# Kernel tuning notes

Hardware: AMD Instinct MI355X
Metric: run time of the kernel (lower is better)

Reference implementation:

```python
import jax, jax.numpy as jnp
import numpy as np

EPS = 1e-6
H = 8  # number of heads


def _ln(x, a, b):
    # Custom LayerNorm from the source: uses unbiased std and divides by (std + eps)
    m = x.mean(-1, keepdims=True)
    s = x.std(-1, keepdims=True, ddof=1)
    return a * (x - m) / (s + EPS) + b


def setup_inputs() -> dict:
    key = jax.random.key(0)
    L, B, S, D, F = 6, 8, 1024, 512, 2048
    ks = jax.random.split(key, 8)
    sc = 0.02  # param init scale
    return {
        "x": jax.random.normal(ks[0], (B, S, D), jnp.float32),
        "mask": jnp.ones((B, 1, S), jnp.int32),
        "Wqkv": (jax.random.normal(ks[1], (L, 4, D, D), jnp.float32) * sc),
        "bqkv": jnp.zeros((L, 4, D), jnp.float32),
        "W1": (jax.random.normal(ks[2], (L, D, F), jnp.float32) * sc),
        "b1": jnp.zeros((L, F), jnp.float32),
        "W2": (jax.random.normal(ks[3], (L, F, D), jnp.float32) * sc),
        "b2": jnp.zeros((L, D), jnp.float32),
        "ln_a": jnp.ones((L, 2, D), jnp.float32),
        "ln_b": jnp.zeros((L, 2, D), jnp.float32),
        "fin_a": jnp.ones((D,), jnp.float32),
        "fin_b": jnp.zeros((D,), jnp.float32),
    }


def reference(x, mask, Wqkv, bqkv, W1, b1, W2, b2, ln_a, ln_b, fin_a, fin_b):
    B, S, D = x.shape
    dk = D // H
    neg_mask = (mask[:, None, :, :] == 0)  # [B,1,1,S] broadcast over heads and queries
    inv_sqrt_dk = 1.0 / jnp.sqrt(jnp.float32(dk))

    def step(h, p):
        Wq, bq, w1, bb1, w2, bb2, la, lb = p
        # --- self-attention sublayer (pre-norm + residual) ---
        y = _ln(h, la[0], lb[0])
        def proj(i):
            return (y @ Wq[i] + bq[i]).reshape(B, S, H, dk).transpose(0, 2, 1, 3)
        q, k, v = proj(0), proj(1), proj(2)
        scores = jnp.einsum('bhqd,bhkd->bhqk', q, k) * inv_sqrt_dk
        scores = jnp.where(neg_mask, jnp.float32(-1e9), scores)
        p_attn = jax.nn.softmax(scores, axis=-1)
        o = jnp.einsum('bhqk,bhkd->bhqd', p_attn, v)
        o = o.transpose(0, 2, 1, 3).reshape(B, S, D)
        h = h + (o @ Wq[3] + bq[3])
        # --- feed-forward sublayer (pre-norm + residual) ---
        y2 = _ln(h, la[1], lb[1])
        h = h + (jax.nn.relu(y2 @ w1 + bb1) @ w2 + bb2)
        return h, None

    out, _ = jax.lax.scan(step, x, (Wqkv, bqkv, W1, b1, W2, b2, ln_a, ln_b))
    return _ln(out, fin_a, fin_b)
```

## Files before the change

kernel.cpp:

```cpp
#include <hip/hip_runtime.h>
#include <stdint.h>

typedef unsigned short u16;
typedef __bf16 bf16x8 __attribute__((ext_vector_type(8)));
typedef float f32x4 __attribute__((ext_vector_type(4)));

__device__ __forceinline__ f32x4 mfma16(bf16x8 a, bf16x8 b, f32x4 c) {
  return __builtin_amdgcn_mfma_f32_16x16x32_bf16(a, b, c, 0, 0, 0);
}

__device__ __forceinline__ void gload_lds16(const void* g, void* l) {
  __builtin_amdgcn_global_load_lds((__attribute__((address_space(1))) void*)g,
                                   (__attribute__((address_space(3))) void*)l,
                                   16, 0, 0);
}

__device__ __forceinline__ u16 f2bf(float f) {
  uint32_t u = __builtin_bit_cast(uint32_t, f);
  u += 0x7fffu + ((u >> 16) & 1u);
  return (u16)(u >> 16);
}
__device__ __forceinline__ uint32_t pack2bf(float lo, float hi) {
  return (uint32_t)f2bf(lo) | ((uint32_t)f2bf(hi) << 16);
}

__global__ void transpose_cast_batch(const float* __restrict__ in,
                                     u16* __restrict__ out, int R, int C) {
  const int z = blockIdx.z;
  in += (size_t)z * R * C;
  out += (size_t)z * R * C;
  __shared__ float tile[32][33];
  const int bx = blockIdx.x * 32, by = blockIdx.y * 32;
  const int tx = threadIdx.x, ty = threadIdx.y;
  for (int i = ty; i < 32; i += 8)
    tile[i][tx] = in[(size_t)(by + i) * C + bx + tx];
  __syncthreads();
  for (int i = ty; i < 32; i += 8)
    out[(size_t)(bx + i) * R + by + tx] = f2bf(tile[tx][i]);
}

template <bool BF16OUT>
__global__ __launch_bounds__(256) void ln_rows(const float* __restrict__ in,
                                               void* __restrict__ out,
                                               const float* __restrict__ ga,
                                               const float* __restrict__ gb) {
  const int row = blockIdx.x, tid = threadIdx.x;
  const float* xr = in + (size_t)row * 512;
  const float x0 = xr[tid], x1 = xr[tid + 256];
  float s = x0 + x1;
#pragma unroll
  for (int off = 32; off > 0; off >>= 1) s += __shfl_down(s, off);
  __shared__ float red[4], red2[4];
  const int wv = tid >> 6, ln = tid & 63;
  if (ln == 0) red[wv] = s;
  __syncthreads();
  const float mean = (red[0] + red[1] + red[2] + red[3]) * (1.0f / 512.0f);
  const float d0 = x0 - mean, d1 = x1 - mean;
  float sq = d0 * d0 + d1 * d1;
#pragma unroll
  for (int off = 32; off > 0; off >>= 1) sq += __shfl_down(sq, off);
  if (ln == 0) red2[wv] = sq;
  __syncthreads();
  const float var = (red2[0] + red2[1] + red2[2] + red2[3]) * (1.0f / 511.0f);
  const float inv = 1.0f / (sqrtf(var) + 1e-6f);
  const float o0 = ga[tid] * d0 * inv + gb[tid];
  const float o1 = ga[tid + 256] * d1 * inv + gb[tid + 256];
  if constexpr (BF16OUT) {
    u16* ob = (u16*)out + (size_t)row * 512;
    ob[tid] = f2bf(o0);
    ob[tid + 256] = f2bf(o1);
  } else {
    float* of = (float*)out + (size_t)row * 512;
    of[tid] = o0;
    of[tid + 256] = o1;
  }
}

template <int EPI>
__global__ __launch_bounds__(256, 2) void gemm_bt(
    const u16* __restrict__ A, const u16* __restrict__ Bt,
    const float* __restrict__ bias, float* __restrict__ hres,
    u16* __restrict__ obf, u16* __restrict__ qout, u16* __restrict__ kout,
    u16* __restrict__ vout, int M, int N, int K) {
  __shared__ __align__(16) u16 sA[2][128 * 64];
  __shared__ __align__(16) u16 sB[2][128 * 64];
  const int tid = threadIdx.x;
  const int wv = tid >> 6, ln = tid & 63;
  const int m0 = blockIdx.y * 128, n0 = blockIdx.x * 128;
  const int wr = (wv >> 1) * 64, wc = (wv & 1) * 64;
  const int l15 = ln & 15, lk8 = (ln >> 4) * 8;

  const f32x4 vzero = {0.f, 0.f, 0.f, 0.f};
  f32x4 acc[4][4];
#pragma unroll
  for (int i = 0; i < 4; ++i)
#pragma unroll
    for (int j = 0; j < 4; ++j) acc[i][j] = vzero;

#define STAGE(bi, k0)                                                          \
  do {                                                                         \
    _Pragma("unroll") for (int it = 0; it < 4; ++it) {                         \
      const int obase = it * 4096 + wv * 1024;                                 \
      const int o = obase + (ln << 4);                                         \
      const int row = o >> 7;                                                  \
      const int scb = (o & 127) ^ ((row & 7) << 4);                            \
      gload_lds16(A + (size_t)(m0 + row) * K + (k0) + (scb >> 1),              \
                  (char*)sA[bi] + obase);                                      \
      gload_lds16(Bt + (size_t)(n0 + row) * K + (k0) + (scb >> 1),             \
                  (char*)sB[bi] + obase);                                      \
    }                                                                          \
  } while (0)

  STAGE(0, 0);
  asm volatile("s_waitcnt vmcnt(0)" ::: "memory");
  __syncthreads();

  int c = 0;
  for (int k0 = 0; k0 < K; k0 += 64) {
    if (k0 + 64 < K) STAGE(c ^ 1, k0 + 64);
#pragma unroll
    for (int kk = 0; kk < 64; kk += 32) {
      bf16x8 af[4], bfr[4];
#pragma unroll
      for (int i = 0; i < 4; ++i) {
        const int ra = wr + i * 16 + l15;
        af[i] = *(const bf16x8*)((const char*)sA[c] + ra * 128 +
                                 (((kk + lk8) << 1) ^ ((ra & 7) << 4)));
        const int rb = wc + i * 16 + l15;
        bfr[i] = *(const bf16x8*)((const char*)sB[c] + rb * 128 +
                                  (((kk + lk8) << 1) ^ ((rb & 7) << 4)));
      }
#pragma unroll
      for (int i = 0; i < 4; ++i)
#pragma unroll
        for (int j = 0; j < 4; ++j) acc[i][j] = mfma16(af[i], bfr[j], acc[i][j]);
    }
    asm volatile("s_waitcnt vmcnt(0)" ::: "memory");
    __syncthreads();
    c ^= 1;
  }
#undef STAGE

#pragma unroll
  for (int i = 0; i < 4; ++i) {
    const int rowb = m0 + wr + i * 16 + ((ln >> 4) << 2);
#pragma unroll
    for (int j = 0; j < 4; ++j) {
      const int col = n0 + wc + j * 16 + l15;
      const float bs = bias[col];
#pragma unroll
      for (int r = 0; r < 4; ++r) {
        const int row = rowb + r;
        const float val = acc[i][j][r] + bs;
        if constexpr (EPI == 0) {
          hres[(size_t)row * N + col] += val;
        } else if constexpr (EPI == 1) {
          obf[(size_t)row * N + col] = f2bf(fmaxf(val, 0.f));
        } else {
          const int b = row >> 10, sidx = row & 1023;
          const int which = col >> 9, hn = col & 511;
          const int hh = hn >> 6, d = hn & 63;
          if (which == 0)
            qout[(((size_t)(b * 8 + hh)) * 1024 + sidx) * 64 + d] = f2bf(val * 0.125f);
          else if (which == 1)
            kout[(((size_t)(b * 8 + hh)) * 1024 + sidx) * 64 + d] = f2bf(val);
          else
            vout[(((size_t)(b * 8 + hh)) * 64 + d) * 1024 + sidx] = f2bf(val);
        }
      }
    }
  }
}

__global__ __launch_bounds__(256) void attn_kernel(
    const u16* __restrict__ q, const u16* __restrict__ k,
    const u16* __restrict__ v, const int* __restrict__ mask,
    u16* __restrict__ o) {
  __shared__ __align__(16) u16 sK[2][64 * 64];
  __shared__ __align__(16) u16 sV[64 * 64];
  __shared__ __align__(16) u16 plds[4][16 * 64];
  __shared__ float sBiasF[1024];

  const int bid = blockIdx.x;
  const int xcd = bid & 7, local = bid >> 3;
  const int bh = xcd * 8 + (local >> 4), qb = local & 15;
  const int b = bh >> 3, hh = bh & 7;
  const int wv = threadIdx.x >> 6, ln = threadIdx.x & 63;
  const int q0 = qb * 64 + wv * 16;
  const u16* qb_p = q + (size_t)bh * 1024 * 64;
  const u16* kb = k + (size_t)bh * 1024 * 64;
  const u16* vb = v + (size_t)bh * 64 * 1024;
  const int* mb = mask + b * 1024;
  const int l15 = ln & 15, g = ln >> 4, g8 = g * 8, g4 = g * 4;
  const int swq = (l15 & 7) << 4;

  {
    const int4 mm = ((const int4*)mb)[threadIdx.x];
    float4 bb;
    bb.x = mm.x ? 0.f : -1e9f;
    bb.y = mm.y ? 0.f : -1e9f;
    bb.z = mm.z ? 0.f : -1e9f;
    bb.w = mm.w ? 0.f : -1e9f;
    ((float4*)sBiasF)[threadIdx.x] = bb;
  }

  bf16x8 aq[2];
  aq[0] = *(const bf16x8*)(qb_p + (size_t)(q0 + l15) * 64 + g8);
  aq[1] = *(const bf16x8*)(qb_p + (size_t)(q0 + l15) * 64 + 32 + g8);

  const f32x4 vzero = {0.f, 0.f, 0.f, 0.f};
  f32x4 accO[4] = {vzero, vzero, vzero, vzero};
  float mrun = -3.0e38f, lrun = 0.f;

#define STAGE_K(bi, t)                                                         \
  do {                                                                         \
    _Pragma("unroll") for (int it = 0; it < 2; ++it) {                         \
      const int obase = (wv * 2 + it) * 1024;                                  \
      const int oo = obase + (ln << 4);                                        \
      const int row = oo >> 7;                                                 \
      const int scb = (oo & 127) ^ ((row & 7) << 4);                           \
      gload_lds16(kb + ((size_t)((t) * 64 + row)) * 64 + (scb >> 1),           \
                  (char*)sK[bi] + obase);                                      \
    }                                                                          \
  } while (0)
#define STAGE_V(t)                                                             \
  do {                                                                         \
    _Pragma("unroll") for (int it = 0; it < 2; ++it) {                         \
      const int obase = (wv * 2 + it) * 1024;                                  \
      const int oo = obase + (ln << 4);                                        \
      const int row = oo >> 7;                                                 \
      const int scb = (oo & 127) ^ ((row & 7) << 4);                           \
      gload_lds16(vb + (size_t)row * 1024 + (t) * 64 + (scb >> 1),             \
                  (char*)sV + obase);                                          \
    }                                                                          \
  } while (0)

  STAGE_K(0, 0);
  STAGE_V(0);
  asm volatile("s_waitcnt vmcnt(0)" ::: "memory");
  __syncthreads();

  for (int t = 0; t < 16; ++t) {
    const int c = t & 1;
    if (t > 0) STAGE_V(t);
    if (t < 15) STAGE_K(c ^ 1, t + 1);
    const int kc = t * 64;

    f32x4 sc4[4];
#pragma unroll
    for (int u = 0; u < 4; ++u) {
      const int row = u * 16 + l15;
      const char* base = (const char*)sK[c] + row * 128;
      const int sw = (row & 7) << 4;
      const bf16x8 k0 = *(const bf16x8*)(base + ((g8 << 1) ^ sw));
      const bf16x8 k1 = *(const bf16x8*)(base + ((64 + (g8 << 1)) ^ sw));
      f32x4 a = *(const f32x4*)(sBiasF + kc + u * 16 + g4);
      a = mfma16(k0, aq[0], a);
      a = mfma16(k1, aq[1], a);
      sc4[u] = a;
    }

    float m16 = sc4[0][0];
#pragma unroll
    for (int u = 0; u < 4; ++u)
#pragma unroll
      for (int r = 0; r < 4; ++r) m16 = fmaxf(m16, sc4[u][r]);
    m16 = fmaxf(m16, __shfl_xor(m16, 16));
    m16 = fmaxf(m16, __shfl_xor(m16, 32));
    const float mnew = fmaxf(mrun, m16);
    const float scale = __expf(mrun - mnew);
    mrun = mnew;
    lrun *= scale;
#pragma unroll
    for (int f = 0; f < 4; ++f) accO[f] *= scale;
    float s = 0.f;
#pragma unroll
    for (int u = 0; u < 4; ++u)
#pragma unroll
      for (int r = 0; r < 4; ++r) {
        const float p = __expf(sc4[u][r] - mnew);
        sc4[u][r] = p;
        s += p;
      }
    s += __shfl_xor(s, 16);
    s += __shfl_xor(s, 32);
    lrun += s;

    char* pw = (char*)plds[wv];
#pragma unroll
    for (int u = 0; u < 4; ++u) {
      uint2 w;
      w.x = pack2bf(sc4[u][0], sc4[u][1]);
      w.y = pack2bf(sc4[u][2], sc4[u][3]);
      *(uint2*)(pw + l15 * 128 + ((u * 32 + g * 8) ^ swq)) = w;
    }
    const bf16x8 ap0 = *(const bf16x8*)(pw + l15 * 128 + ((g8 << 1) ^ swq));
    const bf16x8 ap1 = *(const bf16x8*)(pw + l15 * 128 + ((64 + (g8 << 1)) ^ swq));

    asm volatile("s_waitcnt vmcnt(0)" ::: "memory");

#pragma unroll
    for (int f = 0; f < 4; ++f) {
      const int row = f * 16 + l15;
      const char* vbase = (const char*)sV + row * 128;
      const int sw2 = (row & 7) << 4;
      const bf16x8 v0 = *(const bf16x8*)(vbase + ((g8 << 1) ^ sw2));
      const bf16x8 v1 = *(const bf16x8*)(vbase + ((64 + (g8 << 1)) ^ sw2));
      accO[f] = mfma16(v0, ap0, accO[f]);
      accO[f] = mfma16(v1, ap1, accO[f]);
    }
    __syncthreads();
  }
#undef STAGE_K
#undef STAGE_V

  const float inv = 1.0f / lrun;
  u16* orow = o + ((size_t)(b * 1024 + q0 + l15)) * 512 + hh * 64;
#pragma unroll
  for (int f = 0; f < 4; ++f) {
    uint2 w;
    w.x = pack2bf(accO[f][0] * inv, accO[f][1] * inv);
    w.y = pack2bf(accO[f][2] * inv, accO[f][3] * inv);
    *(uint2*)(orow + f * 16 + g4) = w;
  }
}

extern "C" void kernel_launch(void* const* d_in, const int* in_sizes, int n_in,
                              void* d_out, int out_size, void* d_ws, size_t ws_size,
                              hipStream_t stream) {
  const float* x     = (const float*)d_in[0];
  const int*   mask  = (const int*)d_in[1];
  const float* Wqkv  = (const float*)d_in[2];
  const float* bqkv  = (const float*)d_in[3];
  const float* W1    = (const float*)d_in[4];
  const float* b1    = (const float*)d_in[5];
  const float* W2    = (const float*)d_in[6];
  const float* b2    = (const float*)d_in[7];
  const float* ln_a  = (const float*)d_in[8];
  const float* ln_b  = (const float*)d_in[9];
  const float* fin_a = (const float*)d_in[10];
  const float* fin_b = (const float*)d_in[11];

  const int L = 6;
  const size_t MB = 1u << 20;
  char* ws = (char*)d_ws;
  float* h  = (float*)ws;
  u16* y    = (u16*)(ws + 16 * MB);
  u16* qbuf = (u16*)(ws + 24 * MB);
  u16* kbuf = (u16*)(ws + 32 * MB);
  u16* vbuf = (u16*)(ws + 40 * MB);
  u16* obuf = (u16*)(ws + 48 * MB);
  u16* f1   = (u16*)(ws + 24 * MB);
  u16* wqkvt = (u16*)(ws + 56 * MB);
  u16* w1t  = wqkvt + (size_t)L * 4 * 512 * 512;
  u16* w2t  = w1t + (size_t)L * 2048 * 512;

  hipMemcpyAsync(h, x, (size_t)8192 * 512 * 4, hipMemcpyDeviceToDevice, stream);

  dim3 tb(32, 8);
  transpose_cast_batch<<<dim3(16, 16, 24), tb, 0, stream>>>(Wqkv, wqkvt, 512, 512);
  transpose_cast_batch<<<dim3(64, 16, 6), tb, 0, stream>>>(W1, w1t, 512, 2048);
  transpose_cast_batch<<<dim3(16, 64, 6), tb, 0, stream>>>(W2, w2t, 2048, 512);

  for (int l = 0; l < L; ++l) {
    ln_rows<true><<<8192, 256, 0, stream>>>(h, y, ln_a + (size_t)l * 1024,
                                            ln_b + (size_t)l * 1024);
    gemm_bt<2><<<dim3(12, 64), 256, 0, stream>>>(
        y, wqkvt + (size_t)l * 4 * 512 * 512, bqkv + (size_t)l * 2048, nullptr,
        nullptr, qbuf, kbuf, vbuf, 8192, 1536, 512);
    attn_kernel<<<1024, 256, 0, stream>>>(qbuf, kbuf, vbuf, mask, obuf);
    gemm_bt<0><<<dim3(4, 64), 256, 0, stream>>>(
        obuf, wqkvt + ((size_t)l * 4 + 3) * 512 * 512,
        bqkv + (size_t)l * 2048 + 1536, h, nullptr, nullptr, nullptr, nullptr,
        8192, 512, 512);
    ln_rows<true><<<8192, 256, 0, stream>>>(h, y, ln_a + (size_t)l * 1024 + 512,
                                            ln_b + (size_t)l * 1024 + 512);
    gemm_bt<1><<<dim3(16, 64), 256, 0, stream>>>(
        y, w1t + (size_t)l * 2048 * 512, b1 + (size_t)l * 2048, nullptr, f1,
        nullptr, nullptr, nullptr, 8192, 2048, 512);
    gemm_bt<0><<<dim3(4, 64), 256, 0, stream>>>(
        f1, w2t + (size_t)l * 512 * 2048, b2 + (size_t)l * 512, h, nullptr,
        nullptr, nullptr, nullptr, 8192, 512, 2048);
  }
  ln_rows<false><<<8192, 256, 0, stream>>>(h, d_out, fin_a, fin_b);
}
```

Before: 1.213 ms.

## Split-K the N=512 residual GEMMs with atomics and raise MFMA wave priority

The two residual GEMMs with N=512 (output projection and FFN down-projection) previously launched only 256 blocks. They now use a split-K grid of 2 along z, and each half accumulates into the fp32 residual with atomicAdd; only the first split adds the bias. This is meant to fill more of the GPU's CUs, at the cost of doubled atomic read-modify-write traffic to h and a non-deterministic summation order. The attention kernel also wraps its MFMA sections in s_setprio to favor matrix-issuing waves.

```diff
diff --git a/kernel.cpp b/kernel.cpp
--- a/kernel.cpp
+++ b/kernel.cpp
@@ -76,17 +76,19 @@
   }
 }
 
-template <int EPI>
+template <int EPI, bool SPLITK = false>
 __global__ __launch_bounds__(256, 2) void gemm_bt(
     const u16* __restrict__ A, const u16* __restrict__ Bt,
     const float* __restrict__ bias, float* __restrict__ hres,
     u16* __restrict__ obf, u16* __restrict__ qout, u16* __restrict__ kout,
-    u16* __restrict__ vout, int M, int N, int K) {
+    u16* __restrict__ vout, int M, int N, int K, int kLen) {
   __shared__ __align__(16) u16 sA[2][128 * 64];
   __shared__ __align__(16) u16 sB[2][128 * 64];
   const int tid = threadIdx.x;
   const int wv = tid >> 6, ln = tid & 63;
   const int m0 = blockIdx.y * 128, n0 = blockIdx.x * 128;
+  const int kBase = SPLITK ? blockIdx.z * kLen : 0;
+  const int kEnd = kBase + kLen;
   const int wr = (wv >> 1) * 64, wc = (wv & 1) * 64;
   const int l15 = ln & 15, lk8 = (ln >> 4) * 8;
 
@@ -111,13 +113,13 @@
     }                                                                          \
   } while (0)
 
-  STAGE(0, 0);
+  STAGE(0, kBase);
   asm volatile("s_waitcnt vmcnt(0)" ::: "memory");
   __syncthreads();
 
   int c = 0;
-  for (int k0 = 0; k0 < K; k0 += 64) {
-    if (k0 + 64 < K) STAGE(c ^ 1, k0 + 64);
+  for (int k0 = kBase; k0 < kEnd; k0 += 64) {
+    if (k0 + 64 < kEnd) STAGE(c ^ 1, k0 + 64);
 #pragma unroll
     for (int kk = 0; kk < 64; kk += 32) {
       bf16x8 af[4], bfr[4];
@@ -147,13 +149,16 @@
 #pragma unroll
     for (int j = 0; j < 4; ++j) {
       const int col = n0 + wc + j * 16 + l15;
-      const float bs = bias[col];
+      const float bs = (!SPLITK || blockIdx.z == 0) ? bias[col] : 0.f;
 #pragma unroll
       for (int r = 0; r < 4; ++r) {
         const int row = rowb + r;
         const float val = acc[i][j][r] + bs;
         if constexpr (EPI == 0) {
-          hres[(size_t)row * N + col] += val;
+          if constexpr (SPLITK)
+            atomicAdd(&hres[(size_t)row * N + col], val);
+          else
+            hres[(size_t)row * N + col] += val;
         } else if constexpr (EPI == 1) {
           obf[(size_t)row * N + col] = f2bf(fmaxf(val, 0.f));
         } else {
@@ -247,6 +252,7 @@
     const int kc = t * 64;
 
     f32x4 sc4[4];
+    __builtin_amdgcn_s_setprio(1);
 #pragma unroll
     for (int u = 0; u < 4; ++u) {
       const int row = u * 16 + l15;
@@ -259,6 +265,7 @@
       a = mfma16(k1, aq[1], a);
       sc4[u] = a;
     }
+    __builtin_amdgcn_s_setprio(0);
 
     float m16 = sc4[0][0];
 #pragma unroll
@@ -299,6 +306,7 @@
 
     asm volatile("s_waitcnt vmcnt(0)" ::: "memory");
 
+    __builtin_amdgcn_s_setprio(1);
 #pragma unroll
     for (int f = 0; f < 4; ++f) {
       const int row = f * 16 + l15;
@@ -309,6 +317,7 @@
       accO[f] = mfma16(v0, ap0, accO[f]);
       accO[f] = mfma16(v1, ap1, accO[f]);
     }
+    __builtin_amdgcn_s_setprio(0);
     __syncthreads();
   }
 #undef STAGE_K
@@ -367,20 +376,20 @@
                                             ln_b + (size_t)l * 1024);
     gemm_bt<2><<<dim3(12, 64), 256, 0, stream>>>(
         y, wqkvt + (size_t)l * 4 * 512 * 512, bqkv + (size_t)l * 2048, nullptr,
-        nullptr, qbuf, kbuf, vbuf, 8192, 1536, 512);
+        nullptr, qbuf, kbuf, vbuf, 8192, 1536, 512, 512);
     attn_kernel<<<1024, 256, 0, stream>>>(qbuf, kbuf, vbuf, mask, obuf);
-    gemm_bt<0><<<dim3(4, 64), 256, 0, stream>>>(
+    gemm_bt<0, true><<<dim3(4, 64, 2), 256, 0, stream>>>(
         obuf, wqkvt + ((size_t)l * 4 + 3) * 512 * 512,
         bqkv + (size_t)l * 2048 + 1536, h, nullptr, nullptr, nullptr, nullptr,
-        8192, 512, 512);
+        8192, 512, 512, 256);
     ln_rows<true><<<8192, 256, 0, stream>>>(h, y, ln_a + (size_t)l * 1024 + 512,
                                             ln_b + (size_t)l * 1024 + 512);
     gemm_bt<1><<<dim3(16, 64), 256, 0, stream>>>(
         y, w1t + (size_t)l * 2048 * 512, b1 + (size_t)l * 2048, nullptr, f1,
-        nullptr, nullptr, nullptr, 8192, 2048, 512);
-    gemm_bt<0><<<dim3(4, 64), 256, 0, stream>>>(
+        nullptr, nullptr, nullptr, 8192, 2048, 512, 512);
+    gemm_bt<0, true><<<dim3(4, 64, 2), 256, 0, stream>>>(
         f1, w2t + (size_t)l * 512 * 2048, b2 + (size_t)l * 512, h, nullptr,
-        nullptr, nullptr, nullptr, 8192, 512, 2048);
+        nullptr, nullptr, nullptr, 8192, 512, 2048, 1024);
   }
   ln_rows<false><<<8192, 256, 0, stream>>>(h, d_out, fin_a, fin_b);
 }
```

Result: no change. 1.228 ms (+1.3%).
